# Optimization experiments

Measured on AMD Instinct MI355X. Metric: run time of the kernel, lower is better.

Reference implementation:

```python
import jax, jax.numpy as jnp
import numpy as np

REG = 0.1  # config['reg']


def _poly_filter(s, gammas):
    # Horner evaluation of sum_k gammas[k] * s**k (monomial basis, depth K=len-1).
    out = jnp.full_like(s, gammas[-1])
    for k in range(gammas.shape[0] - 2, -1, -1):
        out = out * s + gammas[k]
    return out


def setup_inputs() -> dict:
    key = jax.random.key(0)
    k1, k2, k3, k4, k5 = jax.random.split(key, 5)
    B, H, N, R = 4, 8, 4096, 64
    U = jax.random.normal(k1, (B, H, N, R), dtype=jnp.float32)
    Sigma = jax.random.normal(k2, (B, H, 1, R), dtype=jnp.float32)
    svd_V = jax.random.normal(k3, (B, H, N, R), dtype=jnp.float32)
    V = jax.random.normal(k4, (B, H, N, R), dtype=jnp.float32)
    mask = jnp.ones((B, N), dtype=jnp.float32)
    # learnable polynomial coefficients; gamma_0 fixed to 1 (fixI=True)
    gammas = jnp.concatenate([jnp.ones((1,), jnp.float32),
                              0.1 * jax.random.normal(k5, (4,), dtype=jnp.float32)])
    return {"U": U, "Sigma": Sigma, "svd_V": svd_V, "V": V, "mask": mask, "gammas": gammas}


def reference(U, Sigma, svd_V, V, mask, gammas):
    # Q: softmax over rank dim r
    Q = jax.nn.softmax(U, axis=-1)                                      # [B,H,N,r]
    # K: masked softmax over sequence dim N
    Kmat = jax.nn.softmax(svd_V - 1e9 * (1.0 - mask[:, None, :, None]), axis=-2)
    S = jax.nn.sigmoid(Sigma)                                           # [B,H,1,r]
    graph_filter = _poly_filter(S, gammas)                              # [B,H,1,r]
    # linear-attention ordering: (Q*filt) @ (K^T @ V), never forms NxN
    KtV = jnp.einsum('bhnr,bhnd->bhrd', Kmat, V)                        # [B,H,r,d]
    X = jnp.einsum('bhnr,bhrd->bhnd', Q * graph_filter, KtV)            # [B,H,N,d]
    r = Q.shape[-1]
    eye = jnp.eye(r, dtype=Q.dtype)
    symQ = jnp.einsum('bhnr,bhns->bhrs', Q, Q) - eye
    ortho_loss = REG * jnp.mean(jnp.abs(symQ), axis=(1, 2, 3))
    symK = jnp.einsum('bhnr,bhns->bhrs', Kmat, Kmat) - eye
    ortho_loss = ortho_loss + REG * jnp.mean(jnp.abs(symK), axis=(1, 2, 3))
    return X, ortho_loss
```

## Files before the change

### kernel.cpp

```cpp
#include <hip/hip_runtime.h>
#include <math.h>

#define NB 4
#define NH 8
#define BHN 32
#define SN 4096
#define RR 64
#define REGC 0.1f

#define MCH 16
#define MROWS 256

typedef short s16x8 __attribute__((ext_vector_type(8)));
typedef float f32x4 __attribute__((ext_vector_type(4)));

__device__ __forceinline__ float wave_sum(float v) {
    #pragma unroll
    for (int off = 32; off; off >>= 1) v += __shfl_xor(v, off, 64);
    return v;
}
__device__ __forceinline__ unsigned short f2bf(float x) {
    unsigned int u = __float_as_uint(x);
    u += 0x7FFFu + ((u >> 16) & 1u);
    return (unsigned short)(u >> 16);
}
__device__ __forceinline__ float bf2f(unsigned short h) {
    return __uint_as_float(((unsigned int)h) << 16);
}
__device__ __forceinline__ unsigned int packbf(float a, float b) {
    return (unsigned int)f2bf(a) | ((unsigned int)f2bf(b) << 16);
}
__device__ __forceinline__ s16x8 ldfrag(const unsigned int* p) {
    uint4 r = *(const uint4*)p;
    return __builtin_bit_cast(s16x8, r);
}
__device__ __forceinline__ int swz(int row, int blk) {
    return (row << 5) + (((blk ^ (row & 7))) << 2);
}
__device__ __forceinline__ void split8(const float* x, uint4& hi, uint4& lo) {
    unsigned short h[8];
    #pragma unroll
    for (int i = 0; i < 8; i++) h[i] = f2bf(x[i]);
    hi = make_uint4((unsigned)h[0] | ((unsigned)h[1] << 16),
                    (unsigned)h[2] | ((unsigned)h[3] << 16),
                    (unsigned)h[4] | ((unsigned)h[5] << 16),
                    (unsigned)h[6] | ((unsigned)h[7] << 16));
    lo = make_uint4(packbf(x[0] - bf2f(h[0]), x[1] - bf2f(h[1])),
                    packbf(x[2] - bf2f(h[2]), x[3] - bf2f(h[3])),
                    packbf(x[4] - bf2f(h[4]), x[5] - bf2f(h[5])),
                    packbf(x[6] - bf2f(h[6]), x[7] - bf2f(h[7])));
}

__global__ void k_zero_loss(float* loss) {
    if (threadIdx.x < NB) loss[threadIdx.x] = 0.0f;
}

#define PT_HI 0
#define PT_LO 2048
#define VT_HI 4096
#define VT_LO 6144
#define QT    8192
__launch_bounds__(512, 4)
__global__ void k_main(const float* __restrict__ U, const float* __restrict__ sv,
                       const float* __restrict__ V, const float* __restrict__ mask,
                       float* __restrict__ ktv_part, float* __restrict__ symk_part,
                       float* __restrict__ symq_part, float* __restrict__ colsum_part) {
    __shared__ __align__(16) unsigned int sm[10240];
    const int chunk = blockIdx.x, bh = blockIdx.y, b = bh >> 3;
    const int t = threadIdx.x, l = t & 63, w = t >> 6;
    const int r15 = l & 15, quad = l >> 4;
    const int ni = w & 3, mi0 = (w >> 2) << 1;
    const size_t rowbase = (size_t)bh * SN * RR;
    const int row0 = chunk * MROWS;

    float csum = 0.0f;
    f32x4 aKV[2], aSK[2], aSQ[2];
    #pragma unroll
    for (int j = 0; j < 2; j++) {
        aKV[j] = (f32x4){0.f, 0.f, 0.f, 0.f};
        aSK[j] = (f32x4){0.f, 0.f, 0.f, 0.f};
        aSQ[j] = (f32x4){0.f, 0.f, 0.f, 0.f};
    }

    float bu[2][8], bx[2][8], bv[2][8];
    #pragma unroll
    for (int i = 0; i < 8; i++) {
        const size_t off = rowbase + (size_t)(row0 + 8 * w + i) * RR + l;
        bu[0][i] = U[off]; bx[0][i] = sv[off]; bv[0][i] = V[off];
    }

    #pragma unroll
    for (int s = 0; s < 4; s++) {
        const int cur = s & 1, nxt = cur ^ 1;
        const int nb = row0 + s * 64;
        float bm[8];
        #pragma unroll
        for (int i = 0; i < 8; i++) bm[i] = mask[b * SN + nb + 8 * w + i];
        float q[8], p[8], vv[8];
        #pragma unroll
        for (int i = 0; i < 8; i++) {
            const float eu = __expf(bu[cur][i]);
            q[i] = eu * (1.0f / wave_sum(eu));
        }
        #pragma unroll
        for (int i = 0; i < 8; i++) {
            p[i] = __expf(bx[cur][i] - 1e9f * (1.0f - bm[i]));
            csum += p[i];
            vv[i] = bv[cur][i];
        }
        if (s < 3) {
            #pragma unroll
            for (int i = 0; i < 8; i++) {
                const size_t off = rowbase + (size_t)(nb + 64 + 8 * w + i) * RR + l;
                bu[nxt][i] = U[off]; bx[nxt][i] = sv[off]; bv[nxt][i] = V[off];
            }
        }
        uint4 ph, pl, vh, vl;
        split8(p, ph, pl);
        split8(vv, vh, vl);
        const uint4 qh = make_uint4(packbf(q[0], q[1]), packbf(q[2], q[3]),
                                    packbf(q[4], q[5]), packbf(q[6], q[7]));
        __syncthreads();
        const int wbase = (l << 5) + ((w ^ (l & 7)) << 2);
        *(uint4*)(sm + PT_HI + wbase) = ph;
        *(uint4*)(sm + PT_LO + wbase) = pl;
        *(uint4*)(sm + VT_HI + wbase) = vh;
        *(uint4*)(sm + VT_LO + wbase) = vl;
        *(uint4*)(sm + QT + wbase) = qh;
        __syncthreads();
        #pragma unroll
        for (int ks = 0; ks < 2; ks++) {
            const int ub = ks * 4 + quad;
            s16x8 Ah[2], Al[2], AQ[2];
            #pragma unroll
            for (int j = 0; j < 2; j++) {
                const int oa = swz((mi0 + j) * 16 + r15, ub);
                Ah[j] = ldfrag(sm + PT_HI + oa);
                Al[j] = ldfrag(sm + PT_LO + oa);
                AQ[j] = ldfrag(sm + QT + oa);
            }
            const int ob = swz(ni * 16 + r15, ub);
            const s16x8 Bvh = ldfrag(sm + VT_HI + ob);
            const s16x8 Bvl = ldfrag(sm + VT_LO + ob);
            const s16x8 Bph = ldfrag(sm + PT_HI + ob);
            const s16x8 Bq  = ldfrag(sm + QT + ob);
            #pragma unroll
            for (int j = 0; j < 2; j++) {
                aKV[j] = __builtin_amdgcn_mfma_f32_16x16x32_bf16(Ah[j], Bvh, aKV[j], 0, 0, 0);
                aKV[j] = __builtin_amdgcn_mfma_f32_16x16x32_bf16(Ah[j], Bvl, aKV[j], 0, 0, 0);
                aKV[j] = __builtin_amdgcn_mfma_f32_16x16x32_bf16(Al[j], Bvh, aKV[j], 0, 0, 0);
                aSK[j] = __builtin_amdgcn_mfma_f32_16x16x32_bf16(Ah[j], Bph, aSK[j], 0, 0, 0);
                aSQ[j] = __builtin_amdgcn_mfma_f32_16x16x32_bf16(AQ[j], Bq,  aSQ[j], 0, 0, 0);
            }
        }
    }
    const size_t pb = ((size_t)bh * MCH + chunk) * 4096;
    #pragma unroll
    for (int j = 0; j < 2; j++)
        #pragma unroll
        for (int r = 0; r < 4; r++) {
            const int e = ((mi0 + j) * 16 + quad * 4 + r) * 64 + ni * 16 + r15;
            ktv_part[pb + e]  = aKV[j][r];
            symk_part[pb + e] = aSK[j][r];
            symq_part[pb + e] = aSQ[j][r];
        }
    __syncthreads();
    float* smf = (float*)sm;
    smf[w * 64 + l] = csum;
    __syncthreads();
    if (w == 0) {
        float scol = 0.f;
        #pragma unroll
        for (int j = 0; j < 8; j++) scol += smf[j * 64 + l];
        colsum_part[(bh * MCH + chunk) * 64 + l] = scol;
    }
}

__global__ void k_finalize(const float* __restrict__ ktv_part, const float* __restrict__ symk_part,
                           const float* __restrict__ symq_part, const float* __restrict__ colsum_part,
                           const float* __restrict__ Sigma, const float* __restrict__ gammas,
                           unsigned short* __restrict__ ktvt_hi, unsigned short* __restrict__ ktvt_lo,
                           float* __restrict__ loss) {
    const int rb = blockIdx.x, bh = blockIdx.y, b = bh >> 3, t = threadIdx.x;
    __shared__ float cs[64];
    if (t < 64) {
        float s = 0.f;
        for (int c = 0; c < MCH; c++) s += colsum_part[(bh * MCH + c) * 64 + t];
        cs[t] = s;
    }
    __syncthreads();
    const float g0 = gammas[0], g1 = gammas[1], g2 = gammas[2], g3 = gammas[3], g4 = gammas[4];
    float lsum = 0.0f;
    #pragma unroll
    for (int o = 0; o < 2; o++) {
        const int idx = rb * 512 + o * 256 + t;
        const int r = idx >> 6, c = idx & 63;
        float kv = 0.f, sk = 0.f, sq = 0.f;
        for (int ch = 0; ch < MCH; ch++) {
            const size_t pb = ((size_t)bh * MCH + ch) * 4096 + idx;
            kv += ktv_part[pb]; sk += symk_part[pb]; sq += symq_part[pb];
        }
        const float iSr = 1.0f / cs[r], iSc = 1.0f / cs[c];
        kv *= iSr;
        sk *= iSr * iSc;
        const float sg = 1.0f / (1.0f + __expf(-Sigma[bh * 64 + r]));
        float f = g4; f = f * sg + g3; f = f * sg + g2; f = f * sg + g1; f = f * sg + g0;
        const float kvf = kv * f;
        const unsigned short h = f2bf(kvf);
        ktvt_hi[bh * 4096 + c * 64 + r] = h;
        ktvt_lo[bh * 4096 + c * 64 + r] = f2bf(kvf - bf2f(h));
        const float eye = (r == c) ? 1.0f : 0.0f;
        lsum += fabsf(sk - eye) + fabsf(sq - eye);
    }
    lsum = wave_sum(lsum);
    __shared__ float smr[4];
    if ((t & 63) == 0) smr[t >> 6] = lsum;
    __syncthreads();
    if (t == 0)
        atomicAdd(loss + b, (REGC / (NH * 64.0f * 64.0f)) * (smr[0] + smr[1] + smr[2] + smr[3]));
}

__launch_bounds__(512, 4)
__global__ void k_xq(const float* __restrict__ U,
                     const unsigned short* __restrict__ ktvt_hi,
                     const unsigned short* __restrict__ ktvt_lo,
                     float* __restrict__ Xout) {
    __shared__ __align__(16) unsigned int sm[4096];
    const int chunk = blockIdx.x, bh = blockIdx.y;
    const int t = threadIdx.x, l = t & 63, w = t >> 6;
    const int r15 = l & 15, quad = l >> 4;
    const int ni = w & 3, mi0 = (w >> 2) << 1;
    const size_t rowbase = (size_t)bh * SN * RR;
    const int row0 = chunk * MROWS;

    s16x8 Bh[2], Bl[2];
    #pragma unroll
    for (int ks = 0; ks < 2; ks++) {
        const int idx = (ni * 16 + r15) * 64 + ks * 32 + quad * 8;
        Bh[ks] = __builtin_bit_cast(s16x8, *(const uint4*)(ktvt_hi + (size_t)bh * 4096 + idx));
        Bl[ks] = __builtin_bit_cast(s16x8, *(const uint4*)(ktvt_lo + (size_t)bh * 4096 + idx));
    }

    float bu[2][8];
    #pragma unroll
    for (int i = 0; i < 8; i++)
        bu[0][i] = U[rowbase + (size_t)(row0 + 8 * w + i) * RR + l];

    #pragma unroll
    for (int s = 0; s < 4; s++) {
        const int cur = s & 1, nxt = cur ^ 1;
        const int nb = row0 + s * 64;
        unsigned int wordv[8];
        const int j = l >> 1;
        #pragma unroll
        for (int i = 0; i < 8; i++) {
            const float eu = __expf(bu[cur][i]);
            const float q = eu * (1.0f / wave_sum(eu));
            const float qn = __shfl_xor(q, 1, 64);
            const unsigned short ah = f2bf(q), nh = f2bf(qn);
            wordv[i] = ((l & 1) == 0)
                ? ((unsigned)ah | ((unsigned)nh << 16))
                : ((unsigned)f2bf(qn - bf2f(nh)) | ((unsigned)f2bf(q - bf2f(ah)) << 16));
        }
        if (s < 3) {
            #pragma unroll
            for (int i = 0; i < 8; i++)
                bu[nxt][i] = U[rowbase + (size_t)(nb + 64 + 8 * w + i) * RR + l];
        }
        __syncthreads();
        #pragma unroll
        for (int i = 0; i < 8; i++) {
            const int nl = 8 * w + i;
            const int addr = (nl << 5) + ((((j >> 2) ^ (nl & 7)) << 2) | (j & 3));
            if ((l & 1) == 0) sm[addr] = wordv[i];
            else              sm[2048 + addr] = wordv[i];
        }
        __syncthreads();
        f32x4 acc[2];
        acc[0] = (f32x4){0.f, 0.f, 0.f, 0.f};
        acc[1] = (f32x4){0.f, 0.f, 0.f, 0.f};
        #pragma unroll
        for (int ks = 0; ks < 2; ks++) {
            #pragma unroll
            for (int jj = 0; jj < 2; jj++) {
                const int oa = swz((mi0 + jj) * 16 + r15, ks * 4 + quad);
                const s16x8 Ah = ldfrag(sm + oa);
                const s16x8 Al = ldfrag(sm + 2048 + oa);
                acc[jj] = __builtin_amdgcn_mfma_f32_16x16x32_bf16(Ah, Bh[ks], acc[jj], 0, 0, 0);
                acc[jj] = __builtin_amdgcn_mfma_f32_16x16x32_bf16(Ah, Bl[ks], acc[jj], 0, 0, 0);
                acc[jj] = __builtin_amdgcn_mfma_f32_16x16x32_bf16(Al, Bh[ks], acc[jj], 0, 0, 0);
            }
        }
        #pragma unroll
        for (int jj = 0; jj < 2; jj++)
            #pragma unroll
            for (int r = 0; r < 4; r++) {
                const int n = nb + (mi0 + jj) * 16 + quad * 4 + r;
                Xout[rowbase + (size_t)n * RR + ni * 16 + r15] = acc[jj][r];
            }
    }
}

extern "C" void kernel_launch(void* const* d_in, const int* in_sizes, int n_in,
                              void* d_out, int out_size, void* d_ws, size_t ws_size,
                              hipStream_t stream) {
    (void)in_sizes; (void)n_in; (void)out_size; (void)ws_size;
    const float* U      = (const float*)d_in[0];
    const float* Sigma  = (const float*)d_in[1];
    const float* sv     = (const float*)d_in[2];
    const float* V      = (const float*)d_in[3];
    const float* mask   = (const float*)d_in[4];
    const float* gammas = (const float*)d_in[5];

    float* X    = (float*)d_out;
    float* loss = X + (size_t)BHN * SN * RR;

    float* ws        = (float*)d_ws;
    float* ktv_part   = ws;
    float* symk_part  = ktv_part + (size_t)BHN * MCH * 4096;
    float* symq_part  = symk_part + (size_t)BHN * MCH * 4096;
    float* colsum_part = symq_part + (size_t)BHN * MCH * 4096;
    unsigned short* ktvt_hi = (unsigned short*)(colsum_part + BHN * MCH * 64);
    unsigned short* ktvt_lo = ktvt_hi + BHN * 4096;

    hipLaunchKernelGGL(k_zero_loss, dim3(1), dim3(64), 0, stream, loss);
    hipLaunchKernelGGL(k_main, dim3(MCH, BHN), dim3(512), 0, stream,
                       U, sv, V, mask, ktv_part, symk_part, symq_part, colsum_part);
    hipLaunchKernelGGL(k_finalize, dim3(8, BHN), dim3(256), 0, stream,
                       ktv_part, symk_part, symq_part, colsum_part, Sigma, gammas,
                       ktvt_hi, ktvt_lo, loss);
    hipLaunchKernelGGL(k_xq, dim3(MCH, BHN), dim3(512), 0, stream,
                       U, ktvt_hi, ktvt_lo, X);
}
```

Baseline: 173.1 us.

## Drop low-order bf16 terms, double-buffer LDS, and split xq into smaller chunks

The P and Q operands are no longer split into hi/lo bf16 pairs, which removes one MFMA per accumulation plus the matching LDS traffic in both k_main and k_xq. The LDS staging is double-buffered by step parity, so the barrier before each write is dropped. k_xq now uses 128-row chunks with twice as many blocks and a higher occupancy hint. Dropping the low-order terms lowers precision of the P·V and Q·KtV products and could exceed the tolerance.

```diff
diff --git a/kernel.cpp b/kernel.cpp
--- a/kernel.cpp
+++ b/kernel.cpp
@@ -10,6 +10,8 @@
 
 #define MCH 16
 #define MROWS 256
+#define XCH 32
+#define XROWS 128
 
 typedef short s16x8 __attribute__((ext_vector_type(8)));
 typedef float f32x4 __attribute__((ext_vector_type(4)));
@@ -55,17 +57,16 @@
     if (threadIdx.x < NB) loss[threadIdx.x] = 0.0f;
 }
 
-#define PT_HI 0
-#define PT_LO 2048
-#define VT_HI 4096
-#define VT_LO 6144
-#define QT    8192
+#define PH 0
+#define VH 2048
+#define VL 4096
+#define QH 6144
 __launch_bounds__(512, 4)
 __global__ void k_main(const float* __restrict__ U, const float* __restrict__ sv,
                        const float* __restrict__ V, const float* __restrict__ mask,
                        float* __restrict__ ktv_part, float* __restrict__ symk_part,
                        float* __restrict__ symq_part, float* __restrict__ colsum_part) {
-    __shared__ __align__(16) unsigned int sm[10240];
+    __shared__ __align__(16) unsigned int sm[16384];
     const int chunk = blockIdx.x, bh = blockIdx.y, b = bh >> 3;
     const int t = threadIdx.x, l = t & 63, w = t >> 6;
     const int r15 = l & 15, quad = l >> 4;
@@ -93,6 +94,7 @@
     for (int s = 0; s < 4; s++) {
         const int cur = s & 1, nxt = cur ^ 1;
         const int nb = row0 + s * 64;
+        const int bufb = (s & 1) * 8192;
         float bm[8];
         #pragma unroll
         for (int i = 0; i < 8; i++) bm[i] = mask[b * SN + nb + 8 * w + i];
@@ -115,40 +117,37 @@
                 bu[nxt][i] = U[off]; bx[nxt][i] = sv[off]; bv[nxt][i] = V[off];
             }
         }
-        uint4 ph, pl, vh, vl;
-        split8(p, ph, pl);
+        uint4 vh, vl;
         split8(vv, vh, vl);
+        const uint4 ph = make_uint4(packbf(p[0], p[1]), packbf(p[2], p[3]),
+                                    packbf(p[4], p[5]), packbf(p[6], p[7]));
         const uint4 qh = make_uint4(packbf(q[0], q[1]), packbf(q[2], q[3]),
                                     packbf(q[4], q[5]), packbf(q[6], q[7]));
-        __syncthreads();
-        const int wbase = (l << 5) + ((w ^ (l & 7)) << 2);
-        *(uint4*)(sm + PT_HI + wbase) = ph;
-        *(uint4*)(sm + PT_LO + wbase) = pl;
-        *(uint4*)(sm + VT_HI + wbase) = vh;
-        *(uint4*)(sm + VT_LO + wbase) = vl;
-        *(uint4*)(sm + QT + wbase) = qh;
+        const int wbase = bufb + (l << 5) + ((w ^ (l & 7)) << 2);
+        *(uint4*)(sm + PH + wbase) = ph;
+        *(uint4*)(sm + VH + wbase) = vh;
+        *(uint4*)(sm + VL + wbase) = vl;
+        *(uint4*)(sm + QH + wbase) = qh;
         __syncthreads();
         #pragma unroll
         for (int ks = 0; ks < 2; ks++) {
             const int ub = ks * 4 + quad;
-            s16x8 Ah[2], Al[2], AQ[2];
+            s16x8 Ah[2], AQ[2];
             #pragma unroll
             for (int j = 0; j < 2; j++) {
-                const int oa = swz((mi0 + j) * 16 + r15, ub);
-                Ah[j] = ldfrag(sm + PT_HI + oa);
-                Al[j] = ldfrag(sm + PT_LO + oa);
-                AQ[j] = ldfrag(sm + QT + oa);
-            }
-            const int ob = swz(ni * 16 + r15, ub);
-            const s16x8 Bvh = ldfrag(sm + VT_HI + ob);
-            const s16x8 Bvl = ldfrag(sm + VT_LO + ob);
-            const s16x8 Bph = ldfrag(sm + PT_HI + ob);
-            const s16x8 Bq  = ldfrag(sm + QT + ob);
+                const int oa = bufb + swz((mi0 + j) * 16 + r15, ub);
+                Ah[j] = ldfrag(sm + PH + oa);
+                AQ[j] = ldfrag(sm + QH + oa);
+            }
+            const int ob = bufb + swz(ni * 16 + r15, ub);
+            const s16x8 Bvh = ldfrag(sm + VH + ob);
+            const s16x8 Bvl = ldfrag(sm + VL + ob);
+            const s16x8 Bph = ldfrag(sm + PH + ob);
+            const s16x8 Bq  = ldfrag(sm + QH + ob);
             #pragma unroll
             for (int j = 0; j < 2; j++) {
                 aKV[j] = __builtin_amdgcn_mfma_f32_16x16x32_bf16(Ah[j], Bvh, aKV[j], 0, 0, 0);
                 aKV[j] = __builtin_amdgcn_mfma_f32_16x16x32_bf16(Ah[j], Bvl, aKV[j], 0, 0, 0);
-                aKV[j] = __builtin_amdgcn_mfma_f32_16x16x32_bf16(Al[j], Bvh, aKV[j], 0, 0, 0);
                 aSK[j] = __builtin_amdgcn_mfma_f32_16x16x32_bf16(Ah[j], Bph, aSK[j], 0, 0, 0);
                 aSQ[j] = __builtin_amdgcn_mfma_f32_16x16x32_bf16(AQ[j], Bq,  aSQ[j], 0, 0, 0);
             }
@@ -220,7 +219,7 @@
         atomicAdd(loss + b, (REGC / (NH * 64.0f * 64.0f)) * (smr[0] + smr[1] + smr[2] + smr[3]));
 }
 
-__launch_bounds__(512, 4)
+__launch_bounds__(512, 8)
 __global__ void k_xq(const float* __restrict__ U,
                      const unsigned short* __restrict__ ktvt_hi,
                      const unsigned short* __restrict__ ktvt_lo,
@@ -231,7 +230,7 @@
     const int r15 = l & 15, quad = l >> 4;
     const int ni = w & 3, mi0 = (w >> 2) << 1;
     const size_t rowbase = (size_t)bh * SN * RR;
-    const int row0 = chunk * MROWS;
+    const int row0 = chunk * XROWS;
 
     s16x8 Bh[2], Bl[2];
     #pragma unroll
@@ -246,34 +245,32 @@
     for (int i = 0; i < 8; i++)
         bu[0][i] = U[rowbase + (size_t)(row0 + 8 * w + i) * RR + l];
 
-    #pragma unroll
-    for (int s = 0; s < 4; s++) {
+    const int jhalf = l >> 1;
+    #pragma unroll
+    for (int s = 0; s < 2; s++) {
         const int cur = s & 1, nxt = cur ^ 1;
         const int nb = row0 + s * 64;
+        const int bufb = (s & 1) * 2048;
         unsigned int wordv[8];
-        const int j = l >> 1;
         #pragma unroll
         for (int i = 0; i < 8; i++) {
             const float eu = __expf(bu[cur][i]);
             const float q = eu * (1.0f / wave_sum(eu));
             const float qn = __shfl_xor(q, 1, 64);
-            const unsigned short ah = f2bf(q), nh = f2bf(qn);
-            wordv[i] = ((l & 1) == 0)
-                ? ((unsigned)ah | ((unsigned)nh << 16))
-                : ((unsigned)f2bf(qn - bf2f(nh)) | ((unsigned)f2bf(q - bf2f(ah)) << 16));
-        }
-        if (s < 3) {
+            wordv[i] = (unsigned)f2bf(q) | ((unsigned)f2bf(qn) << 16);
+        }
+        if (s < 1) {
             #pragma unroll
             for (int i = 0; i < 8; i++)
                 bu[nxt][i] = U[rowbase + (size_t)(nb + 64 + 8 * w + i) * RR + l];
         }
-        __syncthreads();
         #pragma unroll
         for (int i = 0; i < 8; i++) {
-            const int nl = 8 * w + i;
-            const int addr = (nl << 5) + ((((j >> 2) ^ (nl & 7)) << 2) | (j & 3));
-            if ((l & 1) == 0) sm[addr] = wordv[i];
-            else              sm[2048 + addr] = wordv[i];
+            if ((l & 1) == 0) {
+                const int nl = 8 * w + i;
+                const int addr = (nl << 5) + ((((jhalf >> 2) ^ (nl & 7)) << 2) | (jhalf & 3));
+                sm[bufb + addr] = wordv[i];
+            }
         }
         __syncthreads();
         f32x4 acc[2];
@@ -283,12 +280,10 @@
         for (int ks = 0; ks < 2; ks++) {
             #pragma unroll
             for (int jj = 0; jj < 2; jj++) {
-                const int oa = swz((mi0 + jj) * 16 + r15, ks * 4 + quad);
+                const int oa = bufb + swz((mi0 + jj) * 16 + r15, ks * 4 + quad);
                 const s16x8 Ah = ldfrag(sm + oa);
-                const s16x8 Al = ldfrag(sm + 2048 + oa);
                 acc[jj] = __builtin_amdgcn_mfma_f32_16x16x32_bf16(Ah, Bh[ks], acc[jj], 0, 0, 0);
                 acc[jj] = __builtin_amdgcn_mfma_f32_16x16x32_bf16(Ah, Bl[ks], acc[jj], 0, 0, 0);
-                acc[jj] = __builtin_amdgcn_mfma_f32_16x16x32_bf16(Al, Bh[ks], acc[jj], 0, 0, 0);
             }
         }
         #pragma unroll
@@ -315,10 +310,10 @@
     float* X    = (float*)d_out;
     float* loss = X + (size_t)BHN * SN * RR;
 
-    float* ws        = (float*)d_ws;
-    float* ktv_part   = ws;
-    float* symk_part  = ktv_part + (size_t)BHN * MCH * 4096;
-    float* symq_part  = symk_part + (size_t)BHN * MCH * 4096;
+    float* ws          = (float*)d_ws;
+    float* ktv_part    = ws;
+    float* symk_part   = ktv_part + (size_t)BHN * MCH * 4096;
+    float* symq_part   = symk_part + (size_t)BHN * MCH * 4096;
     float* colsum_part = symq_part + (size_t)BHN * MCH * 4096;
     unsigned short* ktvt_hi = (unsigned short*)(colsum_part + BHN * MCH * 64);
     unsigned short* ktvt_lo = ktvt_hi + BHN * 4096;
@@ -329,6 +324,6 @@
     hipLaunchKernelGGL(k_finalize, dim3(8, BHN), dim3(256), 0, stream,
                        ktv_part, symk_part, symq_part, colsum_part, Sigma, gammas,
                        ktvt_hi, ktvt_lo, loss);
-    hipLaunchKernelGGL(k_xq, dim3(MCH, BHN), dim3(512), 0, stream,
+    hipLaunchKernelGGL(k_xq, dim3(XCH, BHN), dim3(512), 0, stream,
                        U, ktvt_hi, ktvt_lo, X);
 }
```

After: 164.9 us. 4.8% less time.
